# Kernel tuning notes

Hardware: AMD Instinct MI355X
Metric: run time of the kernel (lower is better)

## Reference

```python
import jax, jax.numpy as jnp
import numpy as np

EPS = 1e-5  # BatchNorm1d default eps

def _conv1d(x, w, stride, pad):
    # x: [B, Cin, L], w: [Cout, Cin, K]
    return jax.lax.conv_general_dilated(
        x, w, window_strides=(stride,), padding=[(pad, pad)],
        dimension_numbers=('NCH', 'OIH', 'NCH'))

def _bn(x, g, b, m, v):
    # eval-mode BatchNorm1d with running stats; x: [B, C, L]
    scale = g / jnp.sqrt(v + EPS)
    return x * scale[None, :, None] + (b - m * scale)[None, :, None]

def _hardtanh(x):
    return jnp.clip(x, -1.0, 1.0)

def _maxpool2(x):
    B, C, L = x.shape
    return x.reshape(B, C, L // 2, 2).max(axis=-1)


def setup_inputs() -> dict:
    key = jax.random.key(0)
    ks = jax.random.split(key, 20)
    B, L = 256, 16384
    x = jax.random.normal(ks[0], (B, 1, L), dtype=jnp.float32)
    rms = jax.random.uniform(ks[1], (B, 1), dtype=jnp.float32)
    # conv weights (fan-in scaled)
    w1 = jax.random.normal(ks[2], (16, 1, 17), dtype=jnp.float32) * (1.0 / np.sqrt(1 * 17))
    w2 = jax.random.normal(ks[3], (32, 16, 9), dtype=jnp.float32) * (1.0 / np.sqrt(16 * 9))
    w3 = jax.random.normal(ks[4], (64, 32, 5), dtype=jnp.float32) * (1.0 / np.sqrt(32 * 5))
    # batchnorm params (eval mode: gamma, beta, running mean/var)
    def bn_params(k, C):
        k1, k2, k3, k4 = jax.random.split(k, 4)
        g = 1.0 + 0.1 * jax.random.normal(k1, (C,), dtype=jnp.float32)
        b = 0.1 * jax.random.normal(k2, (C,), dtype=jnp.float32)
        m = 0.1 * jax.random.normal(k3, (C,), dtype=jnp.float32)
        v = jax.random.uniform(k4, (C,), dtype=jnp.float32, minval=0.5, maxval=1.5)
        return g, b, m, v
    g1, b1, m1, v1 = bn_params(ks[5], 16)
    g2, b2, m2, v2 = bn_params(ks[6], 32)
    g3, b3, m3, v3 = bn_params(ks[7], 64)
    fc1_w = jax.random.normal(ks[8], (32, 65), dtype=jnp.float32) * (1.0 / np.sqrt(65))
    fc1_b = jnp.zeros((32,), dtype=jnp.float32)
    fc2_w = jax.random.normal(ks[9], (2, 32), dtype=jnp.float32) * (1.0 / np.sqrt(32))
    fc2_b = jnp.zeros((2,), dtype=jnp.float32)
    return dict(x=x, rms=rms, w1=w1, g1=g1, b1=b1, m1=m1, v1=v1,
                w2=w2, g2=g2, b2=b2, m2=m2, v2=v2,
                w3=w3, g3=g3, b3=b3, m3=m3, v3=v3,
                fc1_w=fc1_w, fc1_b=fc1_b, fc2_w=fc2_w, fc2_b=fc2_b)


def reference(x, rms, w1, g1, b1, m1, v1, w2, g2, b2, m2, v2,
              w3, g3, b3, m3, v3, fc1_w, fc1_b, fc2_w, fc2_b):
    # Stage 1: float conv
    h = _conv1d(x, w1, 2, 8)                 # [B,16,8192]
    h = _maxpool2(_hardtanh(_bn(h, g1, b1, m1, v1)))  # [B,16,4096]
    # Stage 2: binarized (sign) weight conv
    h = _conv1d(h, jnp.sign(w2), 2, 4)       # [B,32,2048]
    h = _maxpool2(_hardtanh(_bn(h, g2, b2, m2, v2)))  # [B,32,1024]
    # Stage 3: binarized weight conv
    h = _conv1d(h, jnp.sign(w3), 2, 2)       # [B,64,512]
    h = _maxpool2(_hardtanh(_bn(h, g3, b3, m3, v3)))  # [B,64,256]
    feat = h.mean(axis=-1)                   # AdaptiveAvgPool1d(1) -> [B,64]
    combined = jnp.concatenate([feat, rms], axis=1)   # [B,65]
    h = _hardtanh(combined @ fc1_w.T + fc1_b)
    return h @ fc2_w.T + fc2_b               # [B,2]
```

## Files before the change

kernel.cpp:

```cpp
#include <hip/hip_runtime.h>
#include <hip/hip_bf16.h>

#define EPS 1e-5f

typedef float f32x4 __attribute__((ext_vector_type(4)));
typedef short s16x8 __attribute__((ext_vector_type(8)));

union FragU { uint4 u; s16x8 s; };

__device__ __forceinline__ float ht(float x){ return __builtin_amdgcn_fmed3f(x, -1.f, 1.f); }
__device__ __forceinline__ float sgn(float v){ return (v>0.f)?1.f:((v<0.f)?-1.f:0.f); }
__device__ __forceinline__ unsigned short f2bf(float f){
    unsigned int u = __builtin_bit_cast(unsigned int, f);
    u += 0x7FFFu + ((u>>16)&1u);
    return (unsigned short)(u>>16);
}
__device__ __forceinline__ unsigned pkbf(float a, float b){
    __hip_bfloat162 h = __float22bfloat162_rn(float2{a, b});
    unsigned u;
    __builtin_memcpy(&u, &h, sizeof(u));
    return u;
}

#define DPP_XOR1 0xB1
#define DPP_ROR1 0x121
#define DPP_ROR2 0x122
#define DPP_ROR4 0x124
#define DPP_ROR8 0x128
template<int C>
__device__ __forceinline__ float dppf(float x){
  return __builtin_bit_cast(float, __builtin_amdgcn_update_dpp(
      0, __builtin_bit_cast(int, x), C, 0xF, 0xF, true));
}
__device__ __forceinline__ float poolmax(float r){ return fmaxf(r, dppf<DPP_XOR1>(r)); }
__device__ __forceinline__ float rowsum16(float s){
  s += dppf<DPP_ROR8>(s); s += dppf<DPP_ROR4>(s);
  s += dppf<DPP_ROR2>(s); s += dppf<DPP_ROR1>(s);
  return s;
}

__global__ __launch_bounds__(512) void prep(
    const float* __restrict__ w1, const float* __restrict__ w2, const float* __restrict__ w3,
    const float* g1,const float* b1,const float* m1,const float* v1,
    const float* g2,const float* b2,const float* m2,const float* v2,
    const float* g3,const float* b3,const float* m3,const float* v3,
    unsigned short* __restrict__ a1, unsigned short* __restrict__ a2,
    unsigned short* __restrict__ a3, float* __restrict__ bn){
  const int t = threadIdx.x, bid = blockIdx.x;
  if(bid == 0){
    if(t < 64){
      int q = t>>4, m = t&15;
      #pragma unroll
      for(int j=0;j<8;++j){ int k = 8*q+j;
        a1[t*8+j] = f2bf((k<17)? w1[m*17+k] : 0.f); }
    }
    if(t<16){ float s = g1[t]*rsqrtf(v1[t]+EPS); bn[t]    = s; bn[16+t]  = b1[t]-m1[t]*s; }
    if(t<32){ float s = g2[t]*rsqrtf(v2[t]+EPS); bn[32+t] = s; bn[64+t]  = b2[t]-m2[t]*s; }
    if(t<64){ float s = g3[t]*rsqrtf(v3[t]+EPS); bn[96+t] = s; bn[160+t] = b3[t]-m3[t]*s; }
  } else if(bid <= 2){
    int e = (bid-1)*512 + t;
    if(e < 640){
      int m = e&15, q = (e>>4)&3, hc = e>>6, c = hc%5, h = hc/5;
      int oc = m + 16*h, k = 2*c + (q>>1);
      #pragma unroll
      for(int j=0;j<8;++j){ int ic = 8*(q&1)+j;
        a2[e*8+j] = f2bf((k<9)? sgn(w2[(oc*16+ic)*9+k]) : 0.f); }
    }
  } else {
    int e = (bid-3)*512 + t;
    if(e < 1280){
      int m = e&15, q = (e>>4)&3, gc = e>>6, c = gc%5, g = gc/5;
      int oc = m + 16*g;
      #pragma unroll
      for(int j=0;j<8;++j){ int ic = 8*q+j;
        a3[e*8+j] = f2bf(sgn(w3[(oc*32+ic)*5+c])); }
    }
  }
}

__global__ __launch_bounds__(512, 4) void kfused(const float* __restrict__ x,
    const unsigned short* __restrict__ a1, const unsigned short* __restrict__ a2,
    const unsigned short* __restrict__ a3, const float* __restrict__ bn,
    float* __restrict__ partial){
  __shared__ __align__(16) unsigned short xs[2176];
  __shared__ __align__(16) unsigned short s1[552*24];
  __shared__ __align__(16) unsigned short s2[132*40];
  __shared__ float fws[8*32];
  const int b  = blockIdx.x >> 3;
  const int t  = blockIdx.x & 7;
  const int Q0 = 32*t;
  const int tid = threadIdx.x;
  const int m = tid & 15, q = (tid & 63) >> 4, w = tid >> 6;

  const int x0 = 64*Q0 - 56;
  const float* xrow = &x[b*16384];
  for(int i = tid; i < 544; i += 512){
    int g0 = x0 + 4*i;
    float4 v = make_float4(0.f,0.f,0.f,0.f);
    if(g0 >= 0 && g0 <= 16380) v = *(const float4*)&xrow[g0];
    uint2 pk;
    pk.x = pkbf(v.x, v.y);
    pk.y = pkbf(v.z, v.w);
    *(uint2*)&xs[4*i] = pk;
  }
  FragU af1; af1.u = *(const uint4*)&a1[(q*16+m)*8];
  const float4 sc1 = *(const float4*)&bn[4*q];
  const float4 sh1 = *(const float4*)&bn[16+4*q];
  __syncthreads();

  const unsigned* X32 = (const unsigned*)xs;
  for(int it = 0; it < 9; ++it){
    int tile = it*8 + w;
    if(tile < 67){
      int nl = tile*16 + m;
      int d = nl + 4*q;
      FragU bf;
      bf.u.x = X32[d]; bf.u.y = X32[d+1]; bf.u.z = X32[d+2]; bf.u.w = X32[d+3];
      f32x4 acc = {0.f,0.f,0.f,0.f};
      acc = __builtin_amdgcn_mfma_f32_16x16x32_bf16(af1.s, bf.s, acc, 0,0,0);
      float p0 = poolmax(ht(acc[0]*sc1.x + sh1.x));
      float p1 = poolmax(ht(acc[1]*sc1.y + sh1.y));
      float p2 = poolmax(ht(acc[2]*sc1.z + sh1.z));
      float p3 = poolmax(ht(acc[3]*sc1.w + sh1.w));
      if((m&1)==0){
        int ppl = nl >> 1;
        bool ok = (unsigned)(16*Q0 - 12 + ppl) < 4096u;
        uint2 pk;
        pk.x = ok ? pkbf(p0, p1) : 0u;
        pk.y = ok ? pkbf(p2, p3) : 0u;
        *(uint2*)&s1[ppl*24 + 4*q] = pk;
      }
    }
  }
  __syncthreads();

  FragU af2[2][5];
  #pragma unroll
  for(int h=0;h<2;++h)
    #pragma unroll
    for(int c=0;c<5;++c)
      af2[h][c].u = *(const uint4*)&a2[(((h*5+c)*4+q)*16+m)*8];
  float4 sc2[2], sh2[2];
  #pragma unroll
  for(int h=0;h<2;++h){
    sc2[h] = *(const float4*)&bn[32 + 16*h + 4*q];
    sh2[h] = *(const float4*)&bn[64 + 16*h + 4*q];
  }
  for(int it = 0; it < 3; ++it){
    int tile = it*8 + w;
    if(tile < 17){
      int nl = tile*16 + m;
      f32x4 acc[2] = {{0.f,0.f,0.f,0.f},{0.f,0.f,0.f,0.f}};
      #pragma unroll
      for(int c=0;c<5;++c){
        int row = 2*nl + 2*c + (q>>1);
        FragU bf; bf.u = *(const uint4*)&s1[row*24 + 8*(q&1)];
        acc[0] = __builtin_amdgcn_mfma_f32_16x16x32_bf16(af2[0][c].s, bf.s, acc[0],0,0,0);
        acc[1] = __builtin_amdgcn_mfma_f32_16x16x32_bf16(af2[1][c].s, bf.s, acc[1],0,0,0);
      }
      #pragma unroll
      for(int h=0;h<2;++h){
        float p0 = poolmax(ht(acc[h][0]*sc2[h].x + sh2[h].x));
        float p1 = poolmax(ht(acc[h][1]*sc2[h].y + sh2[h].y));
        float p2 = poolmax(ht(acc[h][2]*sc2[h].z + sh2[h].z));
        float p3 = poolmax(ht(acc[h][3]*sc2[h].w + sh2[h].w));
        if((m&1)==0 && nl < 264){
          int ppl = nl >> 1;
          bool ok = (unsigned)(4*Q0 - 2 + ppl) < 1024u;
          uint2 pk;
          pk.x = ok ? pkbf(p0, p1) : 0u;
          pk.y = ok ? pkbf(p2, p3) : 0u;
          *(uint2*)&s2[ppl*40 + 16*h + 4*q] = pk;
        }
      }
    }
  }
  __syncthreads();

  const int gw = w >> 2, tw = w & 3;
  FragU af3[2][5];
  #pragma unroll
  for(int gl=0;gl<2;++gl)
    #pragma unroll
    for(int c=0;c<5;++c)
      af3[gl][c].u = *(const uint4*)&a3[((((2*gw+gl)*5+c)*4+q)*16+m)*8];
  float4 sc3[2], sh3[2];
  #pragma unroll
  for(int gl=0;gl<2;++gl){
    sc3[gl] = *(const float4*)&bn[96  + 16*(2*gw+gl) + 4*q];
    sh3[gl] = *(const float4*)&bn[160 + 16*(2*gw+gl) + 4*q];
  }
  {
    int nl = tw*16 + m;
    f32x4 acc[2] = {{0.f,0.f,0.f,0.f},{0.f,0.f,0.f,0.f}};
    #pragma unroll
    for(int c=0;c<5;++c){
      int row = 2*nl + c;
      FragU bf; bf.u = *(const uint4*)&s2[row*40 + 8*q];
      acc[0] = __builtin_amdgcn_mfma_f32_16x16x32_bf16(af3[0][c].s, bf.s, acc[0],0,0,0);
      acc[1] = __builtin_amdgcn_mfma_f32_16x16x32_bf16(af3[1][c].s, bf.s, acc[1],0,0,0);
    }
    #pragma unroll
    for(int gl=0;gl<2;++gl){
      float p0 = poolmax(ht(acc[gl][0]*sc3[gl].x + sh3[gl].x));
      float p1 = poolmax(ht(acc[gl][1]*sc3[gl].y + sh3[gl].y));
      float p2 = poolmax(ht(acc[gl][2]*sc3[gl].z + sh3[gl].z));
      float p3 = poolmax(ht(acc[gl][3]*sc3[gl].w + sh3[gl].w));
      float s0 = rowsum16(p0)*0.5f, s1v = rowsum16(p1)*0.5f;
      float s2v = rowsum16(p2)*0.5f, s3 = rowsum16(p3)*0.5f;
      if(m == 0)
        *(float4*)&fws[w*32 + 16*gl + 4*q] = make_float4(s0,s1v,s2v,s3);
    }
  }
  __syncthreads();
  if(tid < 64){
    int ocl = tid & 31;
    int wb  = (tid >> 5) * 4;
    float sum = fws[wb*32+ocl] + fws[(wb+1)*32+ocl] + fws[(wb+2)*32+ocl] + fws[(wb+3)*32+ocl];
    partial[(b*8 + t)*64 + tid] = sum;
  }
}

__global__ __launch_bounds__(64) void kfc(const float* __restrict__ partial,
    const float* __restrict__ rms, const float* __restrict__ fc1w,
    const float* __restrict__ fc1b, const float* __restrict__ fc2w,
    const float* __restrict__ fc2b, float* __restrict__ out){
  __shared__ float feat[64];
  __shared__ float hbuf[32];
  const int b = blockIdx.x, tid = threadIdx.x;
  float s = 0.f;
  #pragma unroll
  for(int t = 0; t < 8; ++t) s += partial[(b*8 + t)*64 + tid];
  feat[tid] = s * (1.f/256.f);
  __syncthreads();
  if(tid < 32){
    float acc = fc1b[tid];
    const float* wv = &fc1w[tid*65];
    #pragma unroll
    for(int c = 0; c < 64; ++c) acc += wv[c]*feat[c];
    acc += wv[64]*rms[b];
    hbuf[tid] = ht(acc);
  }
  __syncthreads();
  if(tid < 2){
    float acc = fc2b[tid];
    const float* wv = &fc2w[tid*32];
    #pragma unroll
    for(int j = 0; j < 32; ++j) acc += wv[j]*hbuf[j];
    out[b*2 + tid] = acc;
  }
}

extern "C" void kernel_launch(void* const* d_in, const int* in_sizes, int n_in,
                              void* d_out, int out_size, void* d_ws, size_t ws_size,
                              hipStream_t stream){
  (void)in_sizes; (void)n_in; (void)out_size; (void)ws_size;
  const float* x    = (const float*)d_in[0];
  const float* rms  = (const float*)d_in[1];
  const float* w1   = (const float*)d_in[2];
  const float* g1   = (const float*)d_in[3];
  const float* b1   = (const float*)d_in[4];
  const float* m1   = (const float*)d_in[5];
  const float* v1   = (const float*)d_in[6];
  const float* w2   = (const float*)d_in[7];
  const float* g2   = (const float*)d_in[8];
  const float* b2   = (const float*)d_in[9];
  const float* m2   = (const float*)d_in[10];
  const float* v2   = (const float*)d_in[11];
  const float* w3   = (const float*)d_in[12];
  const float* g3   = (const float*)d_in[13];
  const float* b3   = (const float*)d_in[14];
  const float* m3   = (const float*)d_in[15];
  const float* v3   = (const float*)d_in[16];
  const float* fc1w = (const float*)d_in[17];
  const float* fc1b = (const float*)d_in[18];
  const float* fc2w = (const float*)d_in[19];
  const float* fc2b = (const float*)d_in[20];
  float* out  = (float*)d_out;

  float*          partial = (float*)d_ws;
  unsigned short* a1  = (unsigned short*)(partial + 131072);
  unsigned short* a2  = a1 + 512;
  unsigned short* a3  = a2 + 5120;
  float*          bnp = (float*)(a3 + 10240);

  prep<<<6,    512, 0, stream>>>(w1, w2, w3, g1,b1,m1,v1, g2,b2,m2,v2, g3,b3,m3,v3,
                                 a1, a2, a3, bnp);
  kfused<<<2048, 512, 0, stream>>>(x, a1, a2, a3, bnp, partial);
  kfc<<<256, 64, 0, stream>>>(partial, rms, fc1w, fc1b, fc2w, fc2b, out);
}
```

Before: 132.4 us.

## Swap MFMA operand order and halve fused block size to 256 threads

Each fused block now covers half as many output positions: 256 threads, 4096 blocks and 16 partials per batch row, so the halo recomputation at tile edges grows relative to useful work. All three MFMA stages swap their A and B operands so the accumulator lanes hold consecutive positions for a single channel. That lets max-pooling run in-lane with fmaxf instead of DPP cross-lane ops, and BN parameters become scalar per lane. The trade-off is scalar 16-bit LDS stores instead of packed uint2 stores, plus extra partial-sum traffic for the final FC kernel.

```diff
diff --git a/kernel.cpp b/kernel.cpp
--- a/kernel.cpp
+++ b/kernel.cpp
@@ -20,23 +20,6 @@
     unsigned u;
     __builtin_memcpy(&u, &h, sizeof(u));
     return u;
-}
-
-#define DPP_XOR1 0xB1
-#define DPP_ROR1 0x121
-#define DPP_ROR2 0x122
-#define DPP_ROR4 0x124
-#define DPP_ROR8 0x128
-template<int C>
-__device__ __forceinline__ float dppf(float x){
-  return __builtin_bit_cast(float, __builtin_amdgcn_update_dpp(
-      0, __builtin_bit_cast(int, x), C, 0xF, 0xF, true));
-}
-__device__ __forceinline__ float poolmax(float r){ return fmaxf(r, dppf<DPP_XOR1>(r)); }
-__device__ __forceinline__ float rowsum16(float s){
-  s += dppf<DPP_ROR8>(s); s += dppf<DPP_ROR4>(s);
-  s += dppf<DPP_ROR2>(s); s += dppf<DPP_ROR1>(s);
-  return s;
 }
 
 __global__ __launch_bounds__(512) void prep(
@@ -78,23 +61,23 @@
   }
 }
 
-__global__ __launch_bounds__(512, 4) void kfused(const float* __restrict__ x,
+__global__ __launch_bounds__(256, 4) void kfused(const float* __restrict__ x,
     const unsigned short* __restrict__ a1, const unsigned short* __restrict__ a2,
     const unsigned short* __restrict__ a3, const float* __restrict__ bn,
     float* __restrict__ partial){
-  __shared__ __align__(16) unsigned short xs[2176];
-  __shared__ __align__(16) unsigned short s1[552*24];
-  __shared__ __align__(16) unsigned short s2[132*40];
-  __shared__ float fws[8*32];
-  const int b  = blockIdx.x >> 3;
-  const int t  = blockIdx.x & 7;
-  const int Q0 = 32*t;
+  __shared__ __align__(16) unsigned short xs[1216];
+  __shared__ __align__(16) unsigned short s1[296*24];
+  __shared__ __align__(16) unsigned short s2[68*40];
+  __shared__ float fws[4*32];
+  const int b  = blockIdx.x >> 4;
+  const int t  = blockIdx.x & 15;
+  const int Q0 = 16*t;
   const int tid = threadIdx.x;
   const int m = tid & 15, q = (tid & 63) >> 4, w = tid >> 6;
 
   const int x0 = 64*Q0 - 56;
   const float* xrow = &x[b*16384];
-  for(int i = tid; i < 544; i += 512){
+  for(int i = tid; i < 304; i += 256){
     int g0 = x0 + 4*i;
     float4 v = make_float4(0.f,0.f,0.f,0.f);
     if(g0 >= 0 && g0 <= 16380) v = *(const float4*)&xrow[g0];
@@ -104,32 +87,29 @@
     *(uint2*)&xs[4*i] = pk;
   }
   FragU af1; af1.u = *(const uint4*)&a1[(q*16+m)*8];
-  const float4 sc1 = *(const float4*)&bn[4*q];
-  const float4 sh1 = *(const float4*)&bn[16+4*q];
+  const float sc1 = bn[m], sh1 = bn[16+m];
   __syncthreads();
 
   const unsigned* X32 = (const unsigned*)xs;
-  for(int it = 0; it < 9; ++it){
-    int tile = it*8 + w;
-    if(tile < 67){
-      int nl = tile*16 + m;
-      int d = nl + 4*q;
+  for(int it = 0; it < 10; ++it){
+    int tile = it*4 + w;
+    if(tile < 37){
+      int d = tile*16 + m + 4*q;
       FragU bf;
       bf.u.x = X32[d]; bf.u.y = X32[d+1]; bf.u.z = X32[d+2]; bf.u.w = X32[d+3];
       f32x4 acc = {0.f,0.f,0.f,0.f};
-      acc = __builtin_amdgcn_mfma_f32_16x16x32_bf16(af1.s, bf.s, acc, 0,0,0);
-      float p0 = poolmax(ht(acc[0]*sc1.x + sh1.x));
-      float p1 = poolmax(ht(acc[1]*sc1.y + sh1.y));
-      float p2 = poolmax(ht(acc[2]*sc1.z + sh1.z));
-      float p3 = poolmax(ht(acc[3]*sc1.w + sh1.w));
-      if((m&1)==0){
-        int ppl = nl >> 1;
-        bool ok = (unsigned)(16*Q0 - 12 + ppl) < 4096u;
-        uint2 pk;
-        pk.x = ok ? pkbf(p0, p1) : 0u;
-        pk.y = ok ? pkbf(p2, p3) : 0u;
-        *(uint2*)&s1[ppl*24 + 4*q] = pk;
-      }
+      acc = __builtin_amdgcn_mfma_f32_16x16x32_bf16(bf.s, af1.s, acc, 0,0,0);
+      float v0 = ht(acc[0]*sc1 + sh1);
+      float v1 = ht(acc[1]*sc1 + sh1);
+      float v2 = ht(acc[2]*sc1 + sh1);
+      float v3 = ht(acc[3]*sc1 + sh1);
+      int ppl = tile*8 + 2*q;
+      int gp  = 16*Q0 - 12 + ppl;
+      float p0 = ((unsigned)gp     < 4096u) ? fmaxf(v0, v1) : 0.f;
+      float p1 = ((unsigned)(gp+1) < 4096u) ? fmaxf(v2, v3) : 0.f;
+      unsigned u = pkbf(p0, p1);
+      s1[ppl*24 + m]     = (unsigned short)u;
+      s1[(ppl+1)*24 + m] = (unsigned short)(u >> 16);
     }
   }
   __syncthreads();
@@ -140,55 +120,58 @@
     #pragma unroll
     for(int c=0;c<5;++c)
       af2[h][c].u = *(const uint4*)&a2[(((h*5+c)*4+q)*16+m)*8];
-  float4 sc2[2], sh2[2];
+  float sc2[2], sh2[2];
   #pragma unroll
   for(int h=0;h<2;++h){
-    sc2[h] = *(const float4*)&bn[32 + 16*h + 4*q];
-    sh2[h] = *(const float4*)&bn[64 + 16*h + 4*q];
+    sc2[h] = bn[32 + m + 16*h];
+    sh2[h] = bn[64 + m + 16*h];
   }
   for(int it = 0; it < 3; ++it){
-    int tile = it*8 + w;
-    if(tile < 17){
+    int tile = it*4 + w;
+    if(tile < 9){
       int nl = tile*16 + m;
       f32x4 acc[2] = {{0.f,0.f,0.f,0.f},{0.f,0.f,0.f,0.f}};
       #pragma unroll
       for(int c=0;c<5;++c){
         int row = 2*nl + 2*c + (q>>1);
         FragU bf; bf.u = *(const uint4*)&s1[row*24 + 8*(q&1)];
-        acc[0] = __builtin_amdgcn_mfma_f32_16x16x32_bf16(af2[0][c].s, bf.s, acc[0],0,0,0);
-        acc[1] = __builtin_amdgcn_mfma_f32_16x16x32_bf16(af2[1][c].s, bf.s, acc[1],0,0,0);
+        acc[0] = __builtin_amdgcn_mfma_f32_16x16x32_bf16(bf.s, af2[0][c].s, acc[0],0,0,0);
+        acc[1] = __builtin_amdgcn_mfma_f32_16x16x32_bf16(bf.s, af2[1][c].s, acc[1],0,0,0);
       }
+      int ppl = tile*8 + 2*q;
+      int gp  = 4*Q0 - 2 + ppl;
+      bool ok0 = (unsigned)gp     < 1024u;
+      bool ok1 = (unsigned)(gp+1) < 1024u;
       #pragma unroll
       for(int h=0;h<2;++h){
-        float p0 = poolmax(ht(acc[h][0]*sc2[h].x + sh2[h].x));
-        float p1 = poolmax(ht(acc[h][1]*sc2[h].y + sh2[h].y));
-        float p2 = poolmax(ht(acc[h][2]*sc2[h].z + sh2[h].z));
-        float p3 = poolmax(ht(acc[h][3]*sc2[h].w + sh2[h].w));
-        if((m&1)==0 && nl < 264){
-          int ppl = nl >> 1;
-          bool ok = (unsigned)(4*Q0 - 2 + ppl) < 1024u;
-          uint2 pk;
-          pk.x = ok ? pkbf(p0, p1) : 0u;
-          pk.y = ok ? pkbf(p2, p3) : 0u;
-          *(uint2*)&s2[ppl*40 + 16*h + 4*q] = pk;
+        float v0 = ht(acc[h][0]*sc2[h] + sh2[h]);
+        float v1 = ht(acc[h][1]*sc2[h] + sh2[h]);
+        float v2 = ht(acc[h][2]*sc2[h] + sh2[h]);
+        float v3 = ht(acc[h][3]*sc2[h] + sh2[h]);
+        float p0 = ok0 ? fmaxf(v0, v1) : 0.f;
+        float p1 = ok1 ? fmaxf(v2, v3) : 0.f;
+        unsigned u = pkbf(p0, p1);
+        if(ppl < 68){
+          s2[ppl*40 + m + 16*h]     = (unsigned short)u;
+          s2[(ppl+1)*40 + m + 16*h] = (unsigned short)(u >> 16);
         }
       }
     }
   }
   __syncthreads();
 
-  const int gw = w >> 2, tw = w & 3;
+  const int tw = w & 1, gw = w >> 1;
   FragU af3[2][5];
   #pragma unroll
   for(int gl=0;gl<2;++gl)
     #pragma unroll
     for(int c=0;c<5;++c)
       af3[gl][c].u = *(const uint4*)&a3[((((2*gw+gl)*5+c)*4+q)*16+m)*8];
-  float4 sc3[2], sh3[2];
+  float sc3[2], sh3[2];
   #pragma unroll
   for(int gl=0;gl<2;++gl){
-    sc3[gl] = *(const float4*)&bn[96  + 16*(2*gw+gl) + 4*q];
-    sh3[gl] = *(const float4*)&bn[160 + 16*(2*gw+gl) + 4*q];
+    sc3[gl] = bn[96  + m + 16*(2*gw+gl)];
+    sh3[gl] = bn[160 + m + 16*(2*gw+gl)];
   }
   {
     int nl = tw*16 + m;
@@ -197,27 +180,26 @@
     for(int c=0;c<5;++c){
       int row = 2*nl + c;
       FragU bf; bf.u = *(const uint4*)&s2[row*40 + 8*q];
-      acc[0] = __builtin_amdgcn_mfma_f32_16x16x32_bf16(af3[0][c].s, bf.s, acc[0],0,0,0);
-      acc[1] = __builtin_amdgcn_mfma_f32_16x16x32_bf16(af3[1][c].s, bf.s, acc[1],0,0,0);
+      acc[0] = __builtin_amdgcn_mfma_f32_16x16x32_bf16(bf.s, af3[0][c].s, acc[0],0,0,0);
+      acc[1] = __builtin_amdgcn_mfma_f32_16x16x32_bf16(bf.s, af3[1][c].s, acc[1],0,0,0);
     }
     #pragma unroll
     for(int gl=0;gl<2;++gl){
-      float p0 = poolmax(ht(acc[gl][0]*sc3[gl].x + sh3[gl].x));
-      float p1 = poolmax(ht(acc[gl][1]*sc3[gl].y + sh3[gl].y));
-      float p2 = poolmax(ht(acc[gl][2]*sc3[gl].z + sh3[gl].z));
-      float p3 = poolmax(ht(acc[gl][3]*sc3[gl].w + sh3[gl].w));
-      float s0 = rowsum16(p0)*0.5f, s1v = rowsum16(p1)*0.5f;
-      float s2v = rowsum16(p2)*0.5f, s3 = rowsum16(p3)*0.5f;
-      if(m == 0)
-        *(float4*)&fws[w*32 + 16*gl + 4*q] = make_float4(s0,s1v,s2v,s3);
+      float v0 = ht(acc[gl][0]*sc3[gl] + sh3[gl]);
+      float v1 = ht(acc[gl][1]*sc3[gl] + sh3[gl]);
+      float v2 = ht(acc[gl][2]*sc3[gl] + sh3[gl]);
+      float v3 = ht(acc[gl][3]*sc3[gl] + sh3[gl]);
+      float sm = fmaxf(v0, v1) + fmaxf(v2, v3);
+      sm += __shfl_xor(sm, 16);
+      sm += __shfl_xor(sm, 32);
+      if(q == 0) fws[w*32 + 16*gl + m] = sm;
     }
   }
   __syncthreads();
   if(tid < 64){
-    int ocl = tid & 31;
-    int wb  = (tid >> 5) * 4;
-    float sum = fws[wb*32+ocl] + fws[(wb+1)*32+ocl] + fws[(wb+2)*32+ocl] + fws[(wb+3)*32+ocl];
-    partial[(b*8 + t)*64 + tid] = sum;
+    int ocl = tid & 31, g = tid >> 5;
+    float sum = fws[(2*g)*32 + ocl] + fws[(2*g+1)*32 + ocl];
+    partial[(b*16 + t)*64 + tid] = sum;
   }
 }
 
@@ -230,7 +212,7 @@
   const int b = blockIdx.x, tid = threadIdx.x;
   float s = 0.f;
   #pragma unroll
-  for(int t = 0; t < 8; ++t) s += partial[(b*8 + t)*64 + tid];
+  for(int t = 0; t < 16; ++t) s += partial[(b*16 + t)*64 + tid];
   feat[tid] = s * (1.f/256.f);
   __syncthreads();
   if(tid < 32){
@@ -279,13 +261,13 @@
   float* out  = (float*)d_out;
 
   float*          partial = (float*)d_ws;
-  unsigned short* a1  = (unsigned short*)(partial + 131072);
+  unsigned short* a1  = (unsigned short*)(partial + 262144);
   unsigned short* a2  = a1 + 512;
   unsigned short* a3  = a2 + 5120;
   float*          bnp = (float*)(a3 + 10240);
 
   prep<<<6,    512, 0, stream>>>(w1, w2, w3, g1,b1,m1,v1, g2,b2,m2,v2, g3,b3,m3,v3,
                                  a1, a2, a3, bnp);
-  kfused<<<2048, 512, 0, stream>>>(x, a1, a2, a3, bnp, partial);
+  kfused<<<4096, 256, 0, stream>>>(x, a1, a2, a3, bnp, partial);
   kfc<<<256, 64, 0, stream>>>(partial, rms, fc1w, fc1b, fc2w, fc2b, out);
 }
```

New measurement: 123.8 us (median of 2 runs). -6.5%, faster.
